# Performance work log

Hardware: AMD Instinct MI355X
Metric: run time of the kernel (lower is better)

The kernel has to match this reference:

```python
import jax, jax.numpy as jnp
import numpy as np

# sizes
N, B, NPG = 8192, 8, 1024          # total nodes, graphs, nodes per graph (equal-size graphs)
D, H, DH, L = 256, 8, 32, 2        # hidden, heads, head dim, layers
IN_C, OUT_D, E, DFF = 128, 64, 262144, 512
EPS = 1e-5


def setup_inputs() -> dict:
    key = jax.random.key(0)
    ks = jax.random.split(key, 20)
    p = lambda i, shp: jax.random.normal(ks[i], shp, jnp.float32) * 0.05
    return dict(
        x=jax.random.normal(ks[0], (N, IN_C), jnp.float32),
        edge_index=jax.random.randint(ks[1], (2, E), 0, N),
        batch=jnp.arange(N, dtype=jnp.int32) // NPG,  # sorted, equal-size graphs
        w_in=p(2, (D, IN_C)), b_in=p(3, (D,)),
        sage_wl=p(4, (L, D, D)), sage_bl=p(5, (L, D)), sage_wr=p(6, (L, D, D)),
        attn_iw=p(7, (L, 3 * D, D)), attn_ib=p(8, (L, 3 * D)),
        attn_ow=p(9, (L, D, D)), attn_ob=p(10, (L, D)),
        n1_w=jnp.ones((L, D)), n1_b=jnp.zeros((L, D)),
        n2_w=jnp.ones((L, D)), n2_b=jnp.zeros((L, D)),
        n3_w=jnp.ones((L, D)), n3_b=jnp.zeros((L, D)),
        mlp_w1=p(11, (L, DFF, D)), mlp_b1=p(12, (L, DFF)),
        mlp_w2=p(13, (L, D, DFF)), mlp_b2=p(14, (L, D)),
        bn_w=jnp.ones((L, D)), bn_b=jnp.zeros((L, D)),
        w_out=p(15, (OUT_D, D)), b_out=p(16, (OUT_D,)),
    )


def _bn(h, w, b):
    # BatchNorm1d over nodes (training-mode batch statistics, biased var)
    m = h.mean(0)
    v = jnp.mean((h - m) ** 2, axis=0)
    return (h - m) * jax.lax.rsqrt(v + EPS) * w + b


def _forward(x, edge_index, batch, w_in, b_in, sage_wl, sage_bl, sage_wr,
             attn_iw, attn_ib, attn_ow, attn_ob, n1_w, n1_b, n2_w, n2_b,
             n3_w, n3_b, mlp_w1, mlp_b1, mlp_w2, mlp_b2, bn_w, bn_b, w_out, b_out):
    src, dst = edge_index[0], edge_index[1]
    deg = jax.ops.segment_sum(jnp.ones((E,), jnp.float32), dst, num_segments=N)
    inv_deg = (1.0 / jnp.clip(deg, 1.0))[:, None]
    scale = 1.0 / np.sqrt(DH)

    h = x @ w_in.T + b_in  # in_proj Linear  [N, D]
    for l in range(L):
        # --- GPSConv: local SAGEConv (mean aggr) + residual + norm1 ---
        agg = jax.ops.segment_sum(h[src], dst, num_segments=N) * inv_deg
        loc = agg @ sage_wl[l].T + sage_bl[l] + h @ sage_wr[l].T
        loc = _bn(loc + h, n1_w[l], n1_b[l])
        # --- GPSConv: dense per-graph multi-head self-attention + residual + norm2 ---
        hd = h.reshape(B, NPG, D)  # to_dense_batch (no padding: equal graph sizes)
        qkv = hd @ attn_iw[l].T + attn_ib[l]  # [B, n, 3D]
        q, k, v = jnp.split(qkv, 3, axis=-1)
        sh = lambda t: t.reshape(B, NPG, H, DH).transpose(0, 2, 1, 3)  # [B, H, n, DH]
        a = jax.nn.softmax(jnp.einsum('bhqd,bhkd->bhqk', sh(q) * scale, sh(k)), axis=-1)
        o = jnp.einsum('bhqk,bhkd->bhqd', a, sh(v)).transpose(0, 2, 1, 3).reshape(B, NPG, D)
        o = (o @ attn_ow[l].T + attn_ob[l]).reshape(N, D)
        glob = _bn(o + h, n2_w[l], n2_b[l])
        # --- GPSConv: sum branches, MLP residual, norm3 ---
        out = loc + glob
        out = out + jax.nn.relu(out @ mlp_w1[l].T + mlp_b1[l]) @ mlp_w2[l].T + mlp_b2[l]
        out = _bn(out, n3_w[l], n3_b[l])
        # --- outer GPS: BatchNorm + relu + (dropout=eval) + residual ---
        h = h + jax.nn.relu(_bn(out, bn_w[l], bn_b[l]))
    pooled = h.reshape(B, NPG, D).mean(axis=1)  # global_mean_pool over sorted equal-size graphs
    return pooled @ w_out.T + b_out  # [B, OUT_D]


def reference(x, edge_index, batch, w_in, b_in, sage_wl, sage_bl, sage_wr,
              attn_iw, attn_ib, attn_ow, attn_ob, n1_w, n1_b, n2_w, n2_b,
              n3_w, n3_b, mlp_w1, mlp_b1, mlp_w2, mlp_b2, bn_w, bn_b, w_out, b_out):
    return _forward(x, edge_index, batch, w_in, b_in, sage_wl, sage_bl, sage_wr,
                    attn_iw, attn_ib, attn_ow, attn_ob, n1_w, n1_b, n2_w, n2_b,
                    n3_w, n3_b, mlp_w1, mlp_b1, mlp_w2, mlp_b2, bn_w, bn_b, w_out, b_out)
```

## Files before the change

### kernel.cpp

```cpp
#include <hip/hip_runtime.h>
#include <hip/hip_bf16.h>

#define N_NODES 8192
#define BGRAPH 8
#define NPG 1024
#define DIM 256
#define NH 8
#define DHEAD 32
#define NLAYERS 2
#define INC 128
#define OUTD 64
#define NEDGE 262144
#define DFF 512
#define EPS 1e-5f

typedef __attribute__((ext_vector_type(4))) float f32x4;
typedef __attribute__((ext_vector_type(8))) short s16x8;
typedef __attribute__((ext_vector_type(4))) ushort u16x4;

__device__ __forceinline__ float b2f(ushort u){
  unsigned v = ((unsigned)u) << 16;
  return __builtin_bit_cast(float, v);
}
__device__ __forceinline__ ushort f2b(float f){
  unsigned u = __builtin_bit_cast(unsigned, f);
  u += 0x7fffu + ((u >> 16) & 1u);
  return (ushort)(u >> 16);
}
__device__ __forceinline__ ushort f2b_trunc(float f){
  return (ushort)(__builtin_bit_cast(unsigned, f) >> 16);
}
__device__ __forceinline__ void gload16(const void* g, void* l){
  __builtin_amdgcn_global_load_lds(
    (const __attribute__((address_space(1))) void*)g,
    (__attribute__((address_space(3))) void*)l,
    16, 0, 0);
}

#define CX  1048576
#define CWI (CX+32768)
#define CSW (CWI+262144)
#define CIW (CSW+393216)
#define COW (CIW+131072)
#define CW1 (COW+262144)
#define CW2 (CW1+262144)
#define NCAST (CW2/256)
__global__ void k_setup(const float* __restrict__ x, const float* __restrict__ w_in,
    const float* __restrict__ wl, const float* __restrict__ wr,
    const float* __restrict__ iw, const float* __restrict__ ow,
    const float* __restrict__ w1, const float* __restrict__ w2,
    ushort* __restrict__ dst, const int* __restrict__ edst, int* __restrict__ deg){
  if(blockIdx.x >= NCAST){
    int i = (blockIdx.x - NCAST)*256 + threadIdx.x;
    int stride = 512*256;
    for(; i<NEDGE; i+=stride) atomicAdd(&deg[edst[i]], 1);
    return;
  }
  int i = blockIdx.x*256 + threadIdx.x;
  float val;
  if(i < CX)       val = x[i];
  else if(i < CWI) val = w_in[i-CX];
  else if(i < CSW){
    int j = i - CWI;
    int l = j >> 17, r = (j >> 9) & 255, k = j & 511;
    val = (k < 256) ? wl[(l<<16) + (r<<8) + k] : wr[(l<<16) + (r<<8) + (k-256)];
  }
  else if(i < CIW) val = iw[i-CSW];
  else if(i < COW) val = ow[i-CIW];
  else if(i < CW1) val = w1[i-COW];
  else             val = w2[i-CW1];
  dst[i] = f2b(val);
}

__global__ void k_scan(const int* __restrict__ deg, int* __restrict__ offs,
                       float* __restrict__ inv_deg){
  __shared__ int s[1024];
  int t = threadIdx.x;
  int base = t*8;
  int loc[8]; int acc=0;
  #pragma unroll
  for(int j=0;j<8;j++){
    int dv = deg[base+j];
    inv_deg[base+j] = 1.0f/(float)(dv>0?dv:1);
    loc[j]=acc; acc += dv;
  }
  s[t]=acc;
  __syncthreads();
  for(int d=1; d<1024; d<<=1){
    int v = (t>=d)? s[t-d] : 0;
    __syncthreads();
    if(t>=d) s[t]+=v;
    __syncthreads();
  }
  int pre = (t>0)? s[t-1] : 0;
  #pragma unroll
  for(int j=0;j<8;j++) offs[base+j] = pre + loc[j];
  if(t==1023) offs[N_NODES] = s[1023];
}
__global__ void k_fill_csr(const int* __restrict__ src, const int* __restrict__ dst,
                           const int* __restrict__ offs, int* __restrict__ cursor,
                           int* __restrict__ csr){
  int i = blockIdx.x*blockDim.x + threadIdx.x;
  int stride = gridDim.x*blockDim.x;
  for(; i<NEDGE; i+=stride){
    int d = dst[i];
    int p = atomicAdd(&cursor[d], 1);
    csr[offs[d]+p] = src[i];
  }
}

__global__ __launch_bounds__(256) void k_aggregate(ushort* __restrict__ hwb,
    const int* __restrict__ offs, const int* __restrict__ csr,
    const float* __restrict__ inv_deg){
  int n = blockIdx.x*4 + (threadIdx.x>>6);
  int lane = threadIdx.x & 63;
  int beg = offs[n], end = offs[n+1];
  f32x4 a0 = {0,0,0,0}, a1 = {0,0,0,0}, a2 = {0,0,0,0}, a3 = {0,0,0,0};
  int i = beg;
  for(; i+4<=end; i+=4){
    int j0=csr[i], j1=csr[i+1], j2=csr[i+2], j3=csr[i+3];
    u16x4 v0 = *(const u16x4*)(hwb + (size_t)j0*512 + 256 + lane*4);
    u16x4 v1 = *(const u16x4*)(hwb + (size_t)j1*512 + 256 + lane*4);
    u16x4 v2 = *(const u16x4*)(hwb + (size_t)j2*512 + 256 + lane*4);
    u16x4 v3 = *(const u16x4*)(hwb + (size_t)j3*512 + 256 + lane*4);
    #pragma unroll
    for(int c=0;c<4;c++){ a0[c]+=b2f(v0[c]); a1[c]+=b2f(v1[c]);
                          a2[c]+=b2f(v2[c]); a3[c]+=b2f(v3[c]); }
  }
  for(; i<end; ++i){
    int j0=csr[i];
    u16x4 v0 = *(const u16x4*)(hwb + (size_t)j0*512 + 256 + lane*4);
    #pragma unroll
    for(int c=0;c<4;c++) a0[c]+=b2f(v0[c]);
  }
  float inv = inv_deg[n];
  u16x4 outv;
  #pragma unroll
  for(int c=0;c<4;c++) outv[c] = f2b((a0[c]+a1[c]+a2[c]+a3[c])*inv);
  *(u16x4*)(hwb + (size_t)n*512 + lane*4) = outv;
}

#define STAGE_AB(t, buf) do{ \
    int kt_ = (t)*64; \
    _Pragma("unroll") \
    for(int it=0; it<2; ++it){ \
      int c = (wave*2+it)*64 + lane; \
      int row = c >> 3, q = c & 7; \
      int qs = q ^ (row & 7); \
      gload16(A + (size_t)(bm+row)*lda + kt_ + qs*8, (char*)As + (buf)*8192 + (wave*2+it)*1024); \
      gload16(W + (size_t)(bn+row)*K   + kt_ + qs*8, (char*)Bs + (buf)*8192 + (wave*2+it)*1024); \
    } \
  }while(0)

template<bool RELU, bool RESID, bool RESIDB, bool BIAS, bool WF32, bool WBF, bool STATS>
__global__ __launch_bounds__(256) void k_mm(const ushort* __restrict__ A,
    const ushort* __restrict__ W, const float* __restrict__ bias,
    const float* __restrict__ resid, const ushort* __restrict__ residb,
    float* __restrict__ Cf, ushort* __restrict__ Cb,
    float* __restrict__ gS, float* __restrict__ gQ,
    int M, int Nc, int K, int lda, int ldcb)
{
  __shared__ ushort As[2*64*64];
  __shared__ ushort Bs[2*64*64];
  __shared__ float sredS[64];
  __shared__ float sredQ[64];
  const int tid = threadIdx.x;
  const int lane = tid & 63, wave = tid >> 6;
  const int l15 = lane & 15, l4 = lane >> 4;
  const int bm = blockIdx.y*64, bn = blockIdx.x*64;
  const int wr = wave >> 1, wc = wave & 1;
  f32x4 acc[2][2] = {};
  const int nt = K >> 6;

  STAGE_AB(0, 0);
  asm volatile("s_waitcnt vmcnt(0)" ::: "memory");
  __builtin_amdgcn_s_barrier();

  int cur = 0;
  for(int t=0; t<nt; ++t){
    if(t+1 < nt) STAGE_AB(t+1, cur^1);
    #pragma unroll
    for(int kk=0; kk<2; ++kk){
      s16x8 af[2], bfr[2];
      #pragma unroll
      for(int mi=0; mi<2; ++mi){
        int row = wr*32 + mi*16 + l15;
        int col = (kk*64 + l4*16) ^ ((row & 7) << 4);
        af[mi] = *(const s16x8*)((const char*)As + cur*8192 + row*128 + col);
      }
      #pragma unroll
      for(int nj=0; nj<2; ++nj){
        int row = wc*32 + nj*16 + l15;
        int col = (kk*64 + l4*16) ^ ((row & 7) << 4);
        bfr[nj] = *(const s16x8*)((const char*)Bs + cur*8192 + row*128 + col);
      }
      #pragma unroll
      for(int mi=0; mi<2; ++mi)
        #pragma unroll
        for(int nj=0; nj<2; ++nj)
          acc[mi][nj] = __builtin_amdgcn_mfma_f32_16x16x32_bf16(af[mi], bfr[nj], acc[mi][nj], 0,0,0);
    }
    asm volatile("s_waitcnt vmcnt(0)" ::: "memory");
    __builtin_amdgcn_s_barrier();
    cur ^= 1;
  }

  float sloc[2] = {0.f,0.f}, qloc[2] = {0.f,0.f};
  #pragma unroll
  for(int mi=0; mi<2; ++mi){
    #pragma unroll
    for(int nj=0; nj<2; ++nj){
      int col = bn + wc*32 + nj*16 + l15;
      float bv = BIAS ? bias[col] : 0.f;
      #pragma unroll
      for(int r=0; r<4; ++r){
        int row = bm + wr*32 + mi*16 + l4*4 + r;
        size_t off = (size_t)row*Nc + col;
        float v = acc[mi][nj][r] + bv;
        if(RESID)  v += resid[off];
        if(RESIDB) v += b2f(residb[off]);
        if(RELU)   v = fmaxf(v, 0.f);
        if(WF32)   Cf[off] = v;
        if(WBF)    Cb[(size_t)row*ldcb + col] = f2b(v);
        if(STATS){ sloc[nj] += v; qloc[nj] += v*v; }
      }
    }
  }
  if(STATS){
    if(tid < 64){ sredS[tid]=0.f; sredQ[tid]=0.f; }
    __syncthreads();
    int c0 = wc*32 + l15;
    atomicAdd(&sredS[c0],    sloc[0]); atomicAdd(&sredQ[c0],    qloc[0]);
    atomicAdd(&sredS[c0+16], sloc[1]); atomicAdd(&sredQ[c0+16], qloc[1]);
    __syncthreads();
    if(tid < 64){
      atomicAdd(&gS[bn+tid], sredS[tid]);
      atomicAdd(&gQ[bn+tid], sredQ[tid]);
    }
  }
}

__global__ __launch_bounds__(256) void k_attn(const ushort* __restrict__ qkv,
                                              ushort* __restrict__ attnO)
{
  __shared__ ushort Ks[3][64*32];
  __shared__ ushort Vt[2][32*64];
  const int tid = threadIdx.x, lane = tid & 63, wave = tid >> 6;
  const int l15 = lane & 15, g = lane >> 4;
  int bid = blockIdx.x;
  int h  = bid & 7;
  int bg = (bid >> 3) & 7;
  int qc = bid >> 6;
  const int nb = bg*NPG + qc*64 + wave*16;
  const int kb = bg*NPG;

  const int rho = tid >> 2, qq = tid & 3;
  const int grp = rho >> 5, r32 = rho & 31;
  const int tt = r32 >> 4, wi = r32 & 15;
  const int jperm = grp*32 + (wi >> 2)*8 + tt*4 + (wi & 3);
  const int qs = qq ^ ((rho >> 1) & 3);

  s16x8 qf = *(const s16x8*)(qkv + (size_t)(nb + l15)*768 + h*32 + g*8);
  {
    const float scale2 = 0.2550370703637335f;
    #pragma unroll
    for(int i=0;i<8;i++) qf[i] = (short)f2b(b2f((ushort)qf[i]) * scale2);
  }
  f32x4 o0 = {0.f,0.f,0.f,0.f}, o1 = {0.f,0.f,0.f,0.f};
  float mrun = -1e30f, lrun = 0.f;

  gload16(qkv + (size_t)(kb + jperm)*768 + 256 + h*32 + qs*8, (char*)Ks[0] + wave*1024);
  s16x8 vcur = *(const s16x8*)(qkv + (size_t)(kb + lane)*768 + 512 + h*32 + wave*8);

  for(int st=0; st<16; ++st){
    int vb = st & 1;
    int kbuf = st % 3;
    #pragma unroll
    for(int i=0;i<8;i++){
      int d = wave*8 + i;
      Vt[vb][d*64 + (lane ^ (i<<3))] = (ushort)vcur[i];
    }
    s16x8 vnext = vcur;
    if(st+1 < 16){
      gload16(qkv + (size_t)(kb + (st+1)*64 + jperm)*768 + 256 + h*32 + qs*8,
              (char*)Ks[(st+1)%3] + wave*1024);
      vnext = *(const s16x8*)(qkv + (size_t)(kb + (st+1)*64 + lane)*768 + 512 + h*32 + wave*8);
    }
    asm volatile("s_waitcnt lgkmcnt(0)" ::: "memory");
    __builtin_amdgcn_s_barrier();

    f32x4 sc[4];
    __builtin_amdgcn_s_setprio(1);
    #pragma unroll
    for(int q4=0; q4<4; ++q4){
      int r0 = q4*16 + l15;
      s16x8 kf = *(const s16x8*)((const char*)Ks[kbuf] + r0*64 + ((g*16) ^ (((r0>>1)&3)<<4)));
      f32x4 z = {0.f,0.f,0.f,0.f};
      sc[q4] = __builtin_amdgcn_mfma_f32_16x16x32_bf16(kf, qf, z, 0,0,0);
    }
    __builtin_amdgcn_s_setprio(0);

    float smax = -1e30f;
    #pragma unroll
    for(int q4=0; q4<4; ++q4)
      #pragma unroll
      for(int r=0; r<4; ++r) smax = fmaxf(smax, sc[q4][r]);
    smax = fmaxf(smax, __shfl_xor(smax, 16));
    smax = fmaxf(smax, __shfl_xor(smax, 32));

    if(!__all((int)(smax <= mrun + 8.0f))){
      float mnew = fmaxf(mrun, smax);
      float alpha = exp2f(mrun - mnew);
      lrun *= alpha;
      #pragma unroll
      for(int r=0;r<4;r++){
        float ar = __shfl(alpha, (lane & 48) | (g*4 + r), 64);
        o0[r] *= ar; o1[r] *= ar;
      }
      mrun = mnew;
    }

    float p[16];
    float ps = 0.f;
    #pragma unroll
    for(int q4=0; q4<4; ++q4)
      #pragma unroll
      for(int r=0; r<4; ++r){
        float pv = exp2f(sc[q4][r] - mrun);
        p[q4*4+r] = pv; ps += pv;
      }
    ps += __shfl_xor(ps, 16);
    ps += __shfl_xor(ps, 32);
    lrun += ps;

    s16x8 pa0, pa1;
    #pragma unroll
    for(int i=0;i<8;i++){ pa0[i] = (short)f2b_trunc(p[i]); pa1[i] = (short)f2b_trunc(p[8+i]); }

    int colb0 = g*16, colb1 = 64 + g*16;
    int d0 = l15, d1 = l15 + 16;
    s16x8 v00 = *(const s16x8*)((const char*)Vt[vb] + d0*128 + (colb0 ^ ((d0&7)<<4)));
    s16x8 v01 = *(const s16x8*)((const char*)Vt[vb] + d1*128 + (colb0 ^ ((d1&7)<<4)));
    s16x8 v10 = *(const s16x8*)((const char*)Vt[vb] + d0*128 + (colb1 ^ ((d0&7)<<4)));
    s16x8 v11 = *(const s16x8*)((const char*)Vt[vb] + d1*128 + (colb1 ^ ((d1&7)<<4)));
    __builtin_amdgcn_s_setprio(1);
    o0 = __builtin_amdgcn_mfma_f32_16x16x32_bf16(pa0, v00, o0, 0,0,0);
    o1 = __builtin_amdgcn_mfma_f32_16x16x32_bf16(pa0, v01, o1, 0,0,0);
    o0 = __builtin_amdgcn_mfma_f32_16x16x32_bf16(pa1, v10, o0, 0,0,0);
    o1 = __builtin_amdgcn_mfma_f32_16x16x32_bf16(pa1, v11, o1, 0,0,0);
    __builtin_amdgcn_s_setprio(0);

    vcur = vnext;
  }
  float inv = 1.0f/lrun;
  #pragma unroll
  for(int r=0;r<4;r++){
    int q2 = g*4 + r;
    float ir = __shfl(inv, (lane & 48) | q2, 64);
    size_t nrow = (size_t)(nb + q2)*DIM + h*32;
    attnO[nrow + l15]      = f2b(o0[r]*ir);
    attnO[nrow + 16 + l15] = f2b(o1[r]*ir);
  }
}

__global__ __launch_bounds__(256) void k_apply12(const ushort* __restrict__ locB,
    const ushort* __restrict__ globB, const float* __restrict__ slot,
    const float* __restrict__ n1w, const float* __restrict__ n1b,
    const float* __restrict__ n2w, const float* __restrict__ n2b,
    ushort* __restrict__ combB){
  int d = threadIdx.x;
  size_t i = (size_t)blockIdx.x*DIM + d;
  const float invn = 1.0f/N_NODES;
  float m1 = slot[d]*invn,     v1 = slot[256+d]*invn - m1*m1;
  float m2 = slot[512+d]*invn, v2 = slot[768+d]*invn - m2*m2;
  float rs1 = rsqrtf(v1+EPS), rs2 = rsqrtf(v2+EPS);
  float y1 = (b2f(locB[i])-m1)*rs1*n1w[d] + n1b[d];
  float y2 = (b2f(globB[i])-m2)*rs2*n2w[d] + n2b[d];
  combB[i] = f2b(y1 + y2);
}

__global__ __launch_bounds__(256) void k_apply3o(const ushort* __restrict__ xB,
    const float* __restrict__ slot, const float* __restrict__ n3w,
    const float* __restrict__ n3b, const float* __restrict__ bw,
    const float* __restrict__ bb, float* __restrict__ H,
    ushort* __restrict__ hwbR){
  int d = threadIdx.x;
  size_t i = (size_t)blockIdx.x*DIM + d;
  const float invn = 1.0f/N_NODES;
  float m   = slot[1024+d]*invn;
  float var = slot[1280+d]*invn - m*m;
  float rs  = rsqrtf(var+EPS);
  float gch = rs*n3w[d];
  float rso = rsqrtf(gch*gch*var + EPS);
  float yo = (b2f(xB[i])-m)*gch*rso*bw[d] + bb[d];
  float h = H[i] + fmaxf(yo, 0.f);
  H[i] = h;
  hwbR[(size_t)blockIdx.x*512 + d] = f2b(h);
}

__global__ void k_pool(const float* __restrict__ h, float* __restrict__ pooled){
  int b = blockIdx.x, c = blockIdx.y, d = threadIdx.x;
  int r0 = c*64;
  float s=0.f;
  for(int i=0;i<64;i++) s += h[(size_t)(b*NPG + r0 + i)*DIM + d];
  atomicAdd(&pooled[b*DIM+d], s*(1.0f/NPG));
}
__global__ void k_out(const float* __restrict__ pooled, const float* __restrict__ w_out,
                      const float* __restrict__ b_out, float* __restrict__ out){
  int t = threadIdx.x;
  if(t >= BGRAPH*OUTD) return;
  int b = t/OUTD, oc = t%OUTD;
  float s = b_out[oc];
  for(int k=0;k<DIM;k++) s += pooled[b*DIM+k]*w_out[oc*DIM+k];
  out[t] = s;
}

extern "C" void kernel_launch(void* const* d_in, const int* in_sizes, int n_in,
                              void* d_out, int out_size, void* d_ws, size_t ws_size,
                              hipStream_t stream) {
  const float* x       = (const float*)d_in[0];
  const int*   edge    = (const int*)d_in[1];
  const float* w_in    = (const float*)d_in[3];
  const float* b_in    = (const float*)d_in[4];
  const float* sage_wl = (const float*)d_in[5];
  const float* sage_bl = (const float*)d_in[6];
  const float* sage_wr = (const float*)d_in[7];
  const float* attn_iw = (const float*)d_in[8];
  const float* attn_ib = (const float*)d_in[9];
  const float* attn_ow = (const float*)d_in[10];
  const float* attn_ob = (const float*)d_in[11];
  const float* n1_w = (const float*)d_in[12];
  const float* n1_b = (const float*)d_in[13];
  const float* n2_w = (const float*)d_in[14];
  const float* n2_b = (const float*)d_in[15];
  const float* n3_w = (const float*)d_in[16];
  const float* n3_b = (const float*)d_in[17];
  const float* mlp_w1 = (const float*)d_in[18];
  const float* mlp_b1 = (const float*)d_in[19];
  const float* mlp_w2 = (const float*)d_in[20];
  const float* mlp_b2 = (const float*)d_in[21];
  const float* bn_w = (const float*)d_in[22];
  const float* bn_b = (const float*)d_in[23];
  const float* w_out = (const float*)d_in[24];
  const float* b_out = (const float*)d_in[25];

  const size_t ND = (size_t)N_NODES*DIM;
  float* ws    = (float*)d_ws;
  float* H     = ws;
  ushort* wsb   = (ushort*)(ws + ND);
  ushort* locB  = wsb;
  ushort* globB = wsb + ND;
  ushort* hwb   = wsb + 2*ND;
  ushort* qkvb  = wsb + 4*ND;
  ushort* attnOb= wsb + 7*ND;
  ushort* combb = wsb + 8*ND;
  ushort* hidb  = wsb + 9*ND;
  ushort* castb = wsb + 11*ND;
  ushort* xb     = castb;
  ushort* w_in_b = castb + CX;
  ushort* sageWb = castb + CWI;
  ushort* iw_b   = castb + CSW;
  ushort* ow_b   = castb + CIW;
  ushort* w1_b   = castb + COW;
  ushort* w2_b   = castb + CW1;
  float* mf      = (float*)(castb + CW2);
  float* inv_deg = mf;
  float* bnslots = mf + 8192;
  float* pooled  = bnslots + 3072;
  int* deg    = (int*)(pooled + 2048);
  int* cursor = deg + N_NODES;
  int* offs   = cursor + N_NODES;
  int* csr    = offs + N_NODES + 8;

  const int* esrc = edge;
  const int* edst = edge + NEDGE;

  hipMemsetAsync(bnslots, 0, (3072+2048)*sizeof(float) + 2*N_NODES*sizeof(int), stream);

  k_setup<<<NCAST+512,256,0,stream>>>(x, w_in, sage_wl, sage_wr, attn_iw,
      attn_ow, mlp_w1, mlp_w2, castb, edst, deg);
  k_scan<<<1,1024,0,stream>>>(deg, offs, inv_deg);
  k_fill_csr<<<512,256,0,stream>>>(esrc, edst, offs, cursor, csr);

  k_mm<false,false,false,true,true,true,false><<<dim3(4,128),256,0,stream>>>(
      xb, w_in_b, b_in, nullptr, nullptr, H, hwb+256, nullptr, nullptr,
      N_NODES, DIM, INC, INC, 512);

  for(int l=0; l<NLAYERS; ++l){
    const ushort* swb = sageWb + (size_t)l*131072;
    const ushort* iwb = iw_b + (size_t)l*196608;
    const ushort* owb = ow_b + (size_t)l*65536;
    const ushort* w1b = w1_b + (size_t)l*131072;
    const ushort* w2b = w2_b + (size_t)l*131072;
    float* slot = bnslots + (size_t)l*1536;

    k_aggregate<<<N_NODES/4,256,0,stream>>>(hwb, offs, csr, inv_deg);
    k_mm<false,true,false,true,false,true,true><<<dim3(4,128),256,0,stream>>>(
        hwb, swb, sage_bl + l*DIM, H, nullptr, nullptr, locB, slot, slot+256,
        N_NODES, DIM, 512, 512, DIM);

    k_mm<false,false,false,true,false,true,false><<<dim3(12,128),256,0,stream>>>(
        hwb+256, iwb, attn_ib + l*3*DIM, nullptr, nullptr, nullptr, qkvb,
        nullptr, nullptr, N_NODES, 3*DIM, DIM, 512, 768);
    k_attn<<<1024,256,0,stream>>>(qkvb, attnOb);
    k_mm<false,true,false,true,false,true,true><<<dim3(4,128),256,0,stream>>>(
        attnOb, owb, attn_ob + l*DIM, H, nullptr, nullptr, globB, slot+512, slot+768,
        N_NODES, DIM, DIM, DIM, DIM);

    k_apply12<<<N_NODES,256,0,stream>>>(locB, globB, slot,
        n1_w + l*DIM, n1_b + l*DIM, n2_w + l*DIM, n2_b + l*DIM, combb);

    k_mm<true,false,false,true,false,true,false><<<dim3(8,128),256,0,stream>>>(
        combb, w1b, mlp_b1 + l*DFF, nullptr, nullptr, nullptr, hidb,
        nullptr, nullptr, N_NODES, DFF, DIM, DIM, 512);
    k_mm<false,false,true,true,false,true,true><<<dim3(4,128),256,0,stream>>>(
        hidb, w2b, mlp_b2 + l*DIM, nullptr, combb, nullptr, globB,
        slot+1024, slot+1280, N_NODES, DIM, 512, 512, DIM);

    k_apply3o<<<N_NODES,256,0,stream>>>(globB, slot, n3_w + l*DIM, n3_b + l*DIM,
        bn_w + l*DIM, bn_b + l*DIM, H, hwb+256);
  }

  k_pool<<<dim3(BGRAPH, NPG/64),256,0,stream>>>(H, pooled);
  k_out<<<1,512,0,stream>>>(pooled, w_out, b_out, (float*)d_out);
}
```

Measured before the change: 306.9 us.

## Merge independent aggregation/QKV and attention/SAGE kernels via block-range dispatch; vectorize BN applies

```diff
diff --git a/kernel.cpp b/kernel.cpp
--- a/kernel.cpp
+++ b/kernel.cpp
@@ -109,37 +109,6 @@
   }
 }
 
-__global__ __launch_bounds__(256) void k_aggregate(ushort* __restrict__ hwb,
-    const int* __restrict__ offs, const int* __restrict__ csr,
-    const float* __restrict__ inv_deg){
-  int n = blockIdx.x*4 + (threadIdx.x>>6);
-  int lane = threadIdx.x & 63;
-  int beg = offs[n], end = offs[n+1];
-  f32x4 a0 = {0,0,0,0}, a1 = {0,0,0,0}, a2 = {0,0,0,0}, a3 = {0,0,0,0};
-  int i = beg;
-  for(; i+4<=end; i+=4){
-    int j0=csr[i], j1=csr[i+1], j2=csr[i+2], j3=csr[i+3];
-    u16x4 v0 = *(const u16x4*)(hwb + (size_t)j0*512 + 256 + lane*4);
-    u16x4 v1 = *(const u16x4*)(hwb + (size_t)j1*512 + 256 + lane*4);
-    u16x4 v2 = *(const u16x4*)(hwb + (size_t)j2*512 + 256 + lane*4);
-    u16x4 v3 = *(const u16x4*)(hwb + (size_t)j3*512 + 256 + lane*4);
-    #pragma unroll
-    for(int c=0;c<4;c++){ a0[c]+=b2f(v0[c]); a1[c]+=b2f(v1[c]);
-                          a2[c]+=b2f(v2[c]); a3[c]+=b2f(v3[c]); }
-  }
-  for(; i<end; ++i){
-    int j0=csr[i];
-    u16x4 v0 = *(const u16x4*)(hwb + (size_t)j0*512 + 256 + lane*4);
-    #pragma unroll
-    for(int c=0;c<4;c++) a0[c]+=b2f(v0[c]);
-  }
-  float inv = inv_deg[n];
-  u16x4 outv;
-  #pragma unroll
-  for(int c=0;c<4;c++) outv[c] = f2b((a0[c]+a1[c]+a2[c]+a3[c])*inv);
-  *(u16x4*)(hwb + (size_t)n*512 + lane*4) = outv;
-}
-
 #define STAGE_AB(t, buf) do{ \
     int kt_ = (t)*64; \
     _Pragma("unroll") \
@@ -151,6 +120,42 @@
       gload16(W + (size_t)(bn+row)*K   + kt_ + qs*8, (char*)Bs + (buf)*8192 + (wave*2+it)*1024); \
     } \
   }while(0)
+
+#define MM_LOOP \
+  f32x4 acc[2][2] = {}; \
+  { const int nt = K >> 6; \
+    STAGE_AB(0, 0); \
+    asm volatile("s_waitcnt vmcnt(0)" ::: "memory"); \
+    __builtin_amdgcn_s_barrier(); \
+    int cur = 0; \
+    for(int t=0; t<nt; ++t){ \
+      if(t+1 < nt) STAGE_AB(t+1, cur^1); \
+      _Pragma("unroll") \
+      for(int kk=0; kk<2; ++kk){ \
+        s16x8 af[2], bfr[2]; \
+        _Pragma("unroll") \
+        for(int mi=0; mi<2; ++mi){ \
+          int row = wr*32 + mi*16 + l15; \
+          int col = (kk*64 + l4*16) ^ ((row & 7) << 4); \
+          af[mi] = *(const s16x8*)((const char*)As + cur*8192 + row*128 + col); \
+        } \
+        _Pragma("unroll") \
+        for(int nj=0; nj<2; ++nj){ \
+          int row = wc*32 + nj*16 + l15; \
+          int col = (kk*64 + l4*16) ^ ((row & 7) << 4); \
+          bfr[nj] = *(const s16x8*)((const char*)Bs + cur*8192 + row*128 + col); \
+        } \
+        _Pragma("unroll") \
+        for(int mi=0; mi<2; ++mi) \
+          _Pragma("unroll") \
+          for(int nj=0; nj<2; ++nj) \
+            acc[mi][nj] = __builtin_amdgcn_mfma_f32_16x16x32_bf16(af[mi], bfr[nj], acc[mi][nj], 0,0,0); \
+      } \
+      asm volatile("s_waitcnt vmcnt(0)" ::: "memory"); \
+      __builtin_amdgcn_s_barrier(); \
+      cur ^= 1; \
+    } \
+  }
 
 template<bool RELU, bool RESID, bool RESIDB, bool BIAS, bool WF32, bool WBF, bool STATS>
 __global__ __launch_bounds__(256) void k_mm(const ushort* __restrict__ A,
@@ -169,41 +174,7 @@
   const int l15 = lane & 15, l4 = lane >> 4;
   const int bm = blockIdx.y*64, bn = blockIdx.x*64;
   const int wr = wave >> 1, wc = wave & 1;
-  f32x4 acc[2][2] = {};
-  const int nt = K >> 6;
-
-  STAGE_AB(0, 0);
-  asm volatile("s_waitcnt vmcnt(0)" ::: "memory");
-  __builtin_amdgcn_s_barrier();
-
-  int cur = 0;
-  for(int t=0; t<nt; ++t){
-    if(t+1 < nt) STAGE_AB(t+1, cur^1);
-    #pragma unroll
-    for(int kk=0; kk<2; ++kk){
-      s16x8 af[2], bfr[2];
-      #pragma unroll
-      for(int mi=0; mi<2; ++mi){
-        int row = wr*32 + mi*16 + l15;
-        int col = (kk*64 + l4*16) ^ ((row & 7) << 4);
-        af[mi] = *(const s16x8*)((const char*)As + cur*8192 + row*128 + col);
-      }
-      #pragma unroll
-      for(int nj=0; nj<2; ++nj){
-        int row = wc*32 + nj*16 + l15;
-        int col = (kk*64 + l4*16) ^ ((row & 7) << 4);
-        bfr[nj] = *(const s16x8*)((const char*)Bs + cur*8192 + row*128 + col);
-      }
-      #pragma unroll
-      for(int mi=0; mi<2; ++mi)
-        #pragma unroll
-        for(int nj=0; nj<2; ++nj)
-          acc[mi][nj] = __builtin_amdgcn_mfma_f32_16x16x32_bf16(af[mi], bfr[nj], acc[mi][nj], 0,0,0);
-    }
-    asm volatile("s_waitcnt vmcnt(0)" ::: "memory");
-    __builtin_amdgcn_s_barrier();
-    cur ^= 1;
-  }
+  MM_LOOP
 
   float sloc[2] = {0.f,0.f}, qloc[2] = {0.f,0.f};
   #pragma unroll
@@ -240,126 +211,239 @@
   }
 }
 
-__global__ __launch_bounds__(256) void k_attn(const ushort* __restrict__ qkv,
-                                              ushort* __restrict__ attnO)
+__global__ __launch_bounds__(256) void k_agg_qkv(ushort* __restrict__ hwb,
+    const int* __restrict__ offs, const int* __restrict__ csr,
+    const float* __restrict__ inv_deg, const ushort* __restrict__ iwb,
+    const float* __restrict__ attn_ib, ushort* __restrict__ qkvb)
 {
-  __shared__ ushort Ks[3][64*32];
-  __shared__ ushort Vt[2][32*64];
-  const int tid = threadIdx.x, lane = tid & 63, wave = tid >> 6;
-  const int l15 = lane & 15, g = lane >> 4;
-  int bid = blockIdx.x;
-  int h  = bid & 7;
-  int bg = (bid >> 3) & 7;
-  int qc = bid >> 6;
-  const int nb = bg*NPG + qc*64 + wave*16;
-  const int kb = bg*NPG;
-
-  const int rho = tid >> 2, qq = tid & 3;
-  const int grp = rho >> 5, r32 = rho & 31;
-  const int tt = r32 >> 4, wi = r32 & 15;
-  const int jperm = grp*32 + (wi >> 2)*8 + tt*4 + (wi & 3);
-  const int qs = qq ^ ((rho >> 1) & 3);
-
-  s16x8 qf = *(const s16x8*)(qkv + (size_t)(nb + l15)*768 + h*32 + g*8);
-  {
-    const float scale2 = 0.2550370703637335f;
+  __shared__ __align__(16) char smem[33280];
+  const int tid = threadIdx.x;
+  const int lane = tid & 63, wave = tid >> 6;
+  if(blockIdx.x < 2048){
+    int n = blockIdx.x*4 + wave;
+    int beg = offs[n], end = offs[n+1];
+    f32x4 a0 = {0,0,0,0}, a1 = {0,0,0,0}, a2 = {0,0,0,0}, a3 = {0,0,0,0};
+    int i = beg;
+    for(; i+4<=end; i+=4){
+      int j0=csr[i], j1=csr[i+1], j2=csr[i+2], j3=csr[i+3];
+      u16x4 v0 = *(const u16x4*)(hwb + (size_t)j0*512 + 256 + lane*4);
+      u16x4 v1 = *(const u16x4*)(hwb + (size_t)j1*512 + 256 + lane*4);
+      u16x4 v2 = *(const u16x4*)(hwb + (size_t)j2*512 + 256 + lane*4);
+      u16x4 v3 = *(const u16x4*)(hwb + (size_t)j3*512 + 256 + lane*4);
+      #pragma unroll
+      for(int c=0;c<4;c++){ a0[c]+=b2f(v0[c]); a1[c]+=b2f(v1[c]);
+                            a2[c]+=b2f(v2[c]); a3[c]+=b2f(v3[c]); }
+    }
+    for(; i<end; ++i){
+      int j0=csr[i];
+      u16x4 v0 = *(const u16x4*)(hwb + (size_t)j0*512 + 256 + lane*4);
+      #pragma unroll
+      for(int c=0;c<4;c++) a0[c]+=b2f(v0[c]);
+    }
+    float inv = inv_deg[n];
+    u16x4 outv;
     #pragma unroll
-    for(int i=0;i<8;i++) qf[i] = (short)f2b(b2f((ushort)qf[i]) * scale2);
-  }
-  f32x4 o0 = {0.f,0.f,0.f,0.f}, o1 = {0.f,0.f,0.f,0.f};
-  float mrun = -1e30f, lrun = 0.f;
-
-  gload16(qkv + (size_t)(kb + jperm)*768 + 256 + h*32 + qs*8, (char*)Ks[0] + wave*1024);
-  s16x8 vcur = *(const s16x8*)(qkv + (size_t)(kb + lane)*768 + 512 + h*32 + wave*8);
-
-  for(int st=0; st<16; ++st){
-    int vb = st & 1;
-    int kbuf = st % 3;
+    for(int c=0;c<4;c++) outv[c] = f2b((a0[c]+a1[c]+a2[c]+a3[c])*inv);
+    *(u16x4*)(hwb + (size_t)n*512 + lane*4) = outv;
+  } else {
+    int idx = blockIdx.x - 2048;
+    const int bn = (idx % 12)*64, bm = (idx / 12)*64;
+    const int l15 = lane & 15, l4 = lane >> 4;
+    const int wr = wave >> 1, wc = wave & 1;
+    const ushort* A = hwb + 256;
+    const ushort* W = iwb;
+    const int K = 256, lda = 512;
+    ushort* As = (ushort*)smem;
+    ushort* Bs = As + 8192;
+    MM_LOOP
     #pragma unroll
-    for(int i=0;i<8;i++){
-      int d = wave*8 + i;
-      Vt[vb][d*64 + (lane ^ (i<<3))] = (ushort)vcur[i];
-    }
-    s16x8 vnext = vcur;
-    if(st+1 < 16){
-      gload16(qkv + (size_t)(kb + (st+1)*64 + jperm)*768 + 256 + h*32 + qs*8,
-              (char*)Ks[(st+1)%3] + wave*1024);
-      vnext = *(const s16x8*)(qkv + (size_t)(kb + (st+1)*64 + lane)*768 + 512 + h*32 + wave*8);
-    }
-    asm volatile("s_waitcnt lgkmcnt(0)" ::: "memory");
-    __builtin_amdgcn_s_barrier();
-
-    f32x4 sc[4];
-    __builtin_amdgcn_s_setprio(1);
+    for(int mi=0; mi<2; ++mi){
+      #pragma unroll
+      for(int nj=0; nj<2; ++nj){
+        int col = bn + wc*32 + nj*16 + l15;
+        float bv = attn_ib[col];
+        #pragma unroll
+        for(int r=0; r<4; ++r){
+          int row = bm + wr*32 + mi*16 + l4*4 + r;
+          qkvb[(size_t)row*768 + col] = f2b(acc[mi][nj][r] + bv);
+        }
+      }
+    }
+  }
+}
+
+__global__ __launch_bounds__(256) void k_attn_sage(const ushort* __restrict__ qkv,
+    ushort* __restrict__ attnO, const ushort* __restrict__ hwb,
+    const ushort* __restrict__ swb, const float* __restrict__ sage_bl,
+    const float* __restrict__ H, ushort* __restrict__ locB,
+    float* __restrict__ gS, float* __restrict__ gQ)
+{
+  __shared__ __align__(16) char smem[33280];
+  const int tid = threadIdx.x;
+  const int lane = tid & 63, wave = tid >> 6;
+  const int l15 = lane & 15;
+  if(blockIdx.x < 1024){
+    ushort* KsB = (ushort*)smem;
+    ushort* VtB = (ushort*)smem + 6144;
+    const int g = lane >> 4;
+    int bid = blockIdx.x;
+    int h  = bid & 7;
+    int bg = (bid >> 3) & 7;
+    int qc = bid >> 6;
+    const int nb = bg*NPG + qc*64 + wave*16;
+    const int kb = bg*NPG;
+
+    const int rho = tid >> 2, qq = tid & 3;
+    const int grp = rho >> 5, r32 = rho & 31;
+    const int tt = r32 >> 4, wi = r32 & 15;
+    const int jperm = grp*32 + (wi >> 2)*8 + tt*4 + (wi & 3);
+    const int qs = qq ^ ((rho >> 1) & 3);
+
+    s16x8 qf = *(const s16x8*)(qkv + (size_t)(nb + l15)*768 + h*32 + g*8);
+    {
+      const float scale2 = 0.2550370703637335f;
+      #pragma unroll
+      for(int i=0;i<8;i++) qf[i] = (short)f2b(b2f((ushort)qf[i]) * scale2);
+    }
+    f32x4 o0 = {0.f,0.f,0.f,0.f}, o1 = {0.f,0.f,0.f,0.f};
+    float mrun = -1e30f, lrun = 0.f;
+
+    gload16(qkv + (size_t)(kb + jperm)*768 + 256 + h*32 + qs*8, (char*)KsB + wave*1024);
+    s16x8 vcur = *(const s16x8*)(qkv + (size_t)(kb + lane)*768 + 512 + h*32 + wave*8);
+
+    for(int st=0; st<16; ++st){
+      int vb = st & 1;
+      int kbuf = st % 3;
+      ushort* vtb = VtB + vb*2048;
+      #pragma unroll
+      for(int i=0;i<8;i++){
+        int d = wave*8 + i;
+        vtb[d*64 + (lane ^ (i<<3))] = (ushort)vcur[i];
+      }
+      s16x8 vnext = vcur;
+      if(st+1 < 16){
+        gload16(qkv + (size_t)(kb + (st+1)*64 + jperm)*768 + 256 + h*32 + qs*8,
+                (char*)(KsB + ((st+1)%3)*2048) + wave*1024);
+        vnext = *(const s16x8*)(qkv + (size_t)(kb + (st+1)*64 + lane)*768 + 512 + h*32 + wave*8);
+      }
+      asm volatile("s_waitcnt lgkmcnt(0)" ::: "memory");
+      __builtin_amdgcn_s_barrier();
+
+      const char* ksb = (const char*)(KsB + kbuf*2048);
+      f32x4 sc[4];
+      __builtin_amdgcn_s_setprio(1);
+      #pragma unroll
+      for(int q4=0; q4<4; ++q4){
+        int r0 = q4*16 + l15;
+        s16x8 kf = *(const s16x8*)(ksb + r0*64 + ((g*16) ^ (((r0>>1)&3)<<4)));
+        f32x4 z = {0.f,0.f,0.f,0.f};
+        sc[q4] = __builtin_amdgcn_mfma_f32_16x16x32_bf16(kf, qf, z, 0,0,0);
+      }
+      __builtin_amdgcn_s_setprio(0);
+
+      float smax = -1e30f;
+      #pragma unroll
+      for(int q4=0; q4<4; ++q4)
+        #pragma unroll
+        for(int r=0; r<4; ++r) smax = fmaxf(smax, sc[q4][r]);
+      smax = fmaxf(smax, __shfl_xor(smax, 16));
+      smax = fmaxf(smax, __shfl_xor(smax, 32));
+
+      if(!__all((int)(smax <= mrun + 8.0f))){
+        float mnew = fmaxf(mrun, smax);
+        float alpha = exp2f(mrun - mnew);
+        lrun *= alpha;
+        #pragma unroll
+        for(int r=0;r<4;r++){
+          float ar = __shfl(alpha, (lane & 48) | (g*4 + r), 64);
+          o0[r] *= ar; o1[r] *= ar;
+        }
+        mrun = mnew;
+      }
+
+      float p[16];
+      float ps = 0.f;
+      #pragma unroll
+      for(int q4=0; q4<4; ++q4)
+        #pragma unroll
+        for(int r=0; r<4; ++r){
+          float pv = exp2f(sc[q4][r] - mrun);
+          p[q4*4+r] = pv; ps += pv;
+        }
+      ps += __shfl_xor(ps, 16);
+      ps += __shfl_xor(ps, 32);
+      lrun += ps;
+
+      s16x8 pa0, pa1;
+      #pragma unroll
+      for(int i=0;i<8;i++){ pa0[i] = (short)f2b_trunc(p[i]); pa1[i] = (short)f2b_trunc(p[8+i]); }
+
+      const char* vtc = (const char*)(VtB + vb*2048);
+      int colb0 = g*16, colb1 = 64 + g*16;
+      int d0 = l15, d1 = l15 + 16;
+      s16x8 v00 = *(const s16x8*)(vtc + d0*128 + (colb0 ^ ((d0&7)<<4)));
+      s16x8 v01 = *(const s16x8*)(vtc + d1*128 + (colb0 ^ ((d1&7)<<4)));
+      s16x8 v10 = *(const s16x8*)(vtc + d0*128 + (colb1 ^ ((d0&7)<<4)));
+      s16x8 v11 = *(const s16x8*)(vtc + d1*128 + (colb1 ^ ((d1&7)<<4)));
+      __builtin_amdgcn_s_setprio(1);
+      o0 = __builtin_amdgcn_mfma_f32_16x16x32_bf16(pa0, v00, o0, 0,0,0);
+      o1 = __builtin_amdgcn_mfma_f32_16x16x32_bf16(pa0, v01, o1, 0,0,0);
+      o0 = __builtin_amdgcn_mfma_f32_16x16x32_bf16(pa1, v10, o0, 0,0,0);
+      o1 = __builtin_amdgcn_mfma_f32_16x16x32_bf16(pa1, v11, o1, 0,0,0);
+      __builtin_amdgcn_s_setprio(0);
+
+      vcur = vnext;
+    }
+    float inv = 1.0f/lrun;
     #pragma unroll
-    for(int q4=0; q4<4; ++q4){
-      int r0 = q4*16 + l15;
-      s16x8 kf = *(const s16x8*)((const char*)Ks[kbuf] + r0*64 + ((g*16) ^ (((r0>>1)&3)<<4)));
-      f32x4 z = {0.f,0.f,0.f,0.f};
-      sc[q4] = __builtin_amdgcn_mfma_f32_16x16x32_bf16(kf, qf, z, 0,0,0);
-    }
-    __builtin_amdgcn_s_setprio(0);
-
-    float smax = -1e30f;
+    for(int r=0;r<4;r++){
+      int q2 = g*4 + r;
+      float ir = __shfl(inv, (lane & 48) | q2, 64);
+      size_t nrow = (size_t)(nb + q2)*DIM + h*32;
+      attnO[nrow + l15]      = f2b(o0[r]*ir);
+      attnO[nrow + 16 + l15] = f2b(o1[r]*ir);
+    }
+  } else {
+    int idx = blockIdx.x - 1024;
+    const int bn = (idx & 3)*64, bm = (idx >> 2)*64;
+    const int l4 = lane >> 4;
+    const int wr = wave >> 1, wc = wave & 1;
+    const ushort* A = hwb;
+    const ushort* W = swb;
+    const int K = 512, lda = 512;
+    ushort* As = (ushort*)smem;
+    ushort* Bs = As + 8192;
+    float* sredS = (float*)(smem + 32768);
+    float* sredQ = sredS + 64;
+    MM_LOOP
+
+    float sloc[2] = {0.f,0.f}, qloc[2] = {0.f,0.f};
     #pragma unroll
-    for(int q4=0; q4<4; ++q4)
-      #pragma unroll
-      for(int r=0; r<4; ++r) smax = fmaxf(smax, sc[q4][r]);
-    smax = fmaxf(smax, __shfl_xor(smax, 16));
-    smax = fmaxf(smax, __shfl_xor(smax, 32));
-
-    if(!__all((int)(smax <= mrun + 8.0f))){
-      float mnew = fmaxf(mrun, smax);
-      float alpha = exp2f(mrun - mnew);
-      lrun *= alpha;
-      #pragma unroll
-      for(int r=0;r<4;r++){
-        float ar = __shfl(alpha, (lane & 48) | (g*4 + r), 64);
-        o0[r] *= ar; o1[r] *= ar;
+    for(int mi=0; mi<2; ++mi){
+      #pragma unroll
+      for(int nj=0; nj<2; ++nj){
+        int col = bn + wc*32 + nj*16 + l15;
+        float bv = sage_bl[col];
+        #pragma unroll
+        for(int r=0; r<4; ++r){
+          int row = bm + wr*32 + mi*16 + l4*4 + r;
+          size_t off = (size_t)row*DIM + col;
+          float v = acc[mi][nj][r] + bv + H[off];
+          locB[off] = f2b(v);
+          sloc[nj] += v; qloc[nj] += v*v;
+        }
       }
-      mrun = mnew;
-    }
-
-    float p[16];
-    float ps = 0.f;
-    #pragma unroll
-    for(int q4=0; q4<4; ++q4)
-      #pragma unroll
-      for(int r=0; r<4; ++r){
-        float pv = exp2f(sc[q4][r] - mrun);
-        p[q4*4+r] = pv; ps += pv;
-      }
-    ps += __shfl_xor(ps, 16);
-    ps += __shfl_xor(ps, 32);
-    lrun += ps;
-
-    s16x8 pa0, pa1;
-    #pragma unroll
-    for(int i=0;i<8;i++){ pa0[i] = (short)f2b_trunc(p[i]); pa1[i] = (short)f2b_trunc(p[8+i]); }
-
-    int colb0 = g*16, colb1 = 64 + g*16;
-    int d0 = l15, d1 = l15 + 16;
-    s16x8 v00 = *(const s16x8*)((const char*)Vt[vb] + d0*128 + (colb0 ^ ((d0&7)<<4)));
-    s16x8 v01 = *(const s16x8*)((const char*)Vt[vb] + d1*128 + (colb0 ^ ((d1&7)<<4)));
-    s16x8 v10 = *(const s16x8*)((const char*)Vt[vb] + d0*128 + (colb1 ^ ((d0&7)<<4)));
-    s16x8 v11 = *(const s16x8*)((const char*)Vt[vb] + d1*128 + (colb1 ^ ((d1&7)<<4)));
-    __builtin_amdgcn_s_setprio(1);
-    o0 = __builtin_amdgcn_mfma_f32_16x16x32_bf16(pa0, v00, o0, 0,0,0);
-    o1 = __builtin_amdgcn_mfma_f32_16x16x32_bf16(pa0, v01, o1, 0,0,0);
-    o0 = __builtin_amdgcn_mfma_f32_16x16x32_bf16(pa1, v10, o0, 0,0,0);
-    o1 = __builtin_amdgcn_mfma_f32_16x16x32_bf16(pa1, v11, o1, 0,0,0);
-    __builtin_amdgcn_s_setprio(0);
-
-    vcur = vnext;
-  }
-  float inv = 1.0f/lrun;
-  #pragma unroll
-  for(int r=0;r<4;r++){
-    int q2 = g*4 + r;
-    float ir = __shfl(inv, (lane & 48) | q2, 64);
-    size_t nrow = (size_t)(nb + q2)*DIM + h*32;
-    attnO[nrow + l15]      = f2b(o0[r]*ir);
-    attnO[nrow + 16 + l15] = f2b(o1[r]*ir);
+    }
+    if(tid < 64){ sredS[tid]=0.f; sredQ[tid]=0.f; }
+    __syncthreads();
+    int c0 = wc*32 + l15;
+    atomicAdd(&sredS[c0],    sloc[0]); atomicAdd(&sredQ[c0],    qloc[0]);
+    atomicAdd(&sredS[c0+16], sloc[1]); atomicAdd(&sredQ[c0+16], qloc[1]);
+    __syncthreads();
+    if(tid < 64){
+      atomicAdd(&gS[bn+tid], sredS[tid]);
+      atomicAdd(&gQ[bn+tid], sredQ[tid]);
+    }
   }
 }
 
@@ -368,34 +452,62 @@
     const float* __restrict__ n1w, const float* __restrict__ n1b,
     const float* __restrict__ n2w, const float* __restrict__ n2b,
     ushort* __restrict__ combB){
-  int d = threadIdx.x;
-  size_t i = (size_t)blockIdx.x*DIM + d;
+  int t = blockIdx.x*256 + threadIdx.x;
+  int base = t*4;
+  int d0 = base & 255;
+  u16x4 lv = *(const u16x4*)(locB + base);
+  u16x4 gv = *(const u16x4*)(globB + base);
+  f32x4 s1 = *(const f32x4*)(slot + d0);
+  f32x4 q1 = *(const f32x4*)(slot + 256 + d0);
+  f32x4 s2 = *(const f32x4*)(slot + 512 + d0);
+  f32x4 q2 = *(const f32x4*)(slot + 768 + d0);
+  f32x4 w1v = *(const f32x4*)(n1w + d0);
+  f32x4 b1v = *(const f32x4*)(n1b + d0);
+  f32x4 w2v = *(const f32x4*)(n2w + d0);
+  f32x4 b2v = *(const f32x4*)(n2b + d0);
   const float invn = 1.0f/N_NODES;
-  float m1 = slot[d]*invn,     v1 = slot[256+d]*invn - m1*m1;
-  float m2 = slot[512+d]*invn, v2 = slot[768+d]*invn - m2*m2;
-  float rs1 = rsqrtf(v1+EPS), rs2 = rsqrtf(v2+EPS);
-  float y1 = (b2f(locB[i])-m1)*rs1*n1w[d] + n1b[d];
-  float y2 = (b2f(globB[i])-m2)*rs2*n2w[d] + n2b[d];
-  combB[i] = f2b(y1 + y2);
+  u16x4 outv;
+  #pragma unroll
+  for(int c=0;c<4;c++){
+    float m1 = s1[c]*invn, v1 = q1[c]*invn - m1*m1;
+    float m2 = s2[c]*invn, v2 = q2[c]*invn - m2*m2;
+    float y1 = (b2f(lv[c])-m1)*rsqrtf(v1+EPS)*w1v[c] + b1v[c];
+    float y2 = (b2f(gv[c])-m2)*rsqrtf(v2+EPS)*w2v[c] + b2v[c];
+    outv[c] = f2b(y1 + y2);
+  }
+  *(u16x4*)(combB + base) = outv;
 }
 
 __global__ __launch_bounds__(256) void k_apply3o(const ushort* __restrict__ xB,
     const float* __restrict__ slot, const float* __restrict__ n3w,
-    const float* __restrict__ n3b, const float* __restrict__ bw,
-    const float* __restrict__ bb, float* __restrict__ H,
-    ushort* __restrict__ hwbR){
-  int d = threadIdx.x;
-  size_t i = (size_t)blockIdx.x*DIM + d;
+    const float* __restrict__ bw, const float* __restrict__ bb,
+    float* __restrict__ H, ushort* __restrict__ hwbR){
+  int t = blockIdx.x*256 + threadIdx.x;
+  int base = t*4;
+  int d0 = base & 255;
+  int row = base >> 8;
+  u16x4 xv = *(const u16x4*)(xB + base);
+  f32x4 s3 = *(const f32x4*)(slot + 1024 + d0);
+  f32x4 q3 = *(const f32x4*)(slot + 1280 + d0);
+  f32x4 wv3 = *(const f32x4*)(n3w + d0);
+  f32x4 bwv = *(const f32x4*)(bw + d0);
+  f32x4 bbv = *(const f32x4*)(bb + d0);
+  f32x4 hv = *(f32x4*)(H + base);
   const float invn = 1.0f/N_NODES;
-  float m   = slot[1024+d]*invn;
-  float var = slot[1280+d]*invn - m*m;
-  float rs  = rsqrtf(var+EPS);
-  float gch = rs*n3w[d];
-  float rso = rsqrtf(gch*gch*var + EPS);
-  float yo = (b2f(xB[i])-m)*gch*rso*bw[d] + bb[d];
-  float h = H[i] + fmaxf(yo, 0.f);
-  H[i] = h;
-  hwbR[(size_t)blockIdx.x*512 + d] = f2b(h);
+  u16x4 outv;
+  #pragma unroll
+  for(int c=0;c<4;c++){
+    float m = s3[c]*invn, var = q3[c]*invn - m*m;
+    float rs = rsqrtf(var+EPS);
+    float gch = rs*wv3[c];
+    float rso = rsqrtf(gch*gch*var + EPS);
+    float yo = (b2f(xv[c])-m)*gch*rso*bwv[c] + bbv[c];
+    float h = hv[c] + fmaxf(yo, 0.f);
+    hv[c] = h;
+    outv[c] = f2b(h);
+  }
+  *(f32x4*)(H + base) = hv;
+  *(u16x4*)(hwbR + (size_t)row*512 + d0) = outv;
 }
 
 __global__ void k_pool(const float* __restrict__ h, float* __restrict__ pooled){
@@ -494,20 +606,17 @@
     const ushort* w2b = w2_b + (size_t)l*131072;
     float* slot = bnslots + (size_t)l*1536;
 
-    k_aggregate<<<N_NODES/4,256,0,stream>>>(hwb, offs, csr, inv_deg);
-    k_mm<false,true,false,true,false,true,true><<<dim3(4,128),256,0,stream>>>(
-        hwb, swb, sage_bl + l*DIM, H, nullptr, nullptr, locB, slot, slot+256,
-        N_NODES, DIM, 512, 512, DIM);
-
-    k_mm<false,false,false,true,false,true,false><<<dim3(12,128),256,0,stream>>>(
-        hwb+256, iwb, attn_ib + l*3*DIM, nullptr, nullptr, nullptr, qkvb,
-        nullptr, nullptr, N_NODES, 3*DIM, DIM, 512, 768);
-    k_attn<<<1024,256,0,stream>>>(qkvb, attnOb);
+    k_agg_qkv<<<3584,256,0,stream>>>(hwb, offs, csr, inv_deg, iwb,
+        attn_ib + l*3*DIM, qkvb);
+
+    k_attn_sage<<<1536,256,0,stream>>>(qkvb, attnOb, hwb, swb,
+        sage_bl + l*DIM, H, locB, slot, slot+256);
+
     k_mm<false,true,false,true,false,true,true><<<dim3(4,128),256,0,stream>>>(
         attnOb, owb, attn_ob + l*DIM, H, nullptr, nullptr, globB, slot+512, slot+768,
         N_NODES, DIM, DIM, DIM, DIM);
 
-    k_apply12<<<N_NODES,256,0,stream>>>(locB, globB, slot,
+    k_apply12<<<2048,256,0,stream>>>(locB, globB, slot,
         n1_w + l*DIM, n1_b + l*DIM, n2_w + l*DIM, n2_b + l*DIM, combb);
 
     k_mm<true,false,false,true,false,true,false><<<dim3(8,128),256,0,stream>>>(
@@ -517,7 +626,7 @@
         hidb, w2b, mlp_b2 + l*DIM, nullptr, combb, nullptr, globB,
         slot+1024, slot+1280, N_NODES, DIM, 512, 512, DIM);
 
-    k_apply3o<<<N_NODES,256,0,stream>>>(globB, slot, n3_w + l*DIM, n3_b + l*DIM,
+    k_apply3o<<<2048,256,0,stream>>>(globB, slot, n3_w + l*DIM,
         bn_w + l*DIM, bn_b + l*DIM, H, hwb+256);
   }
 
```

Result: faster. 282.0 us (-8.1%).
